# Optimization experiments

Measured on AMD Instinct MI355X. Metric: run time of the kernel, lower is better.

## Reference

```python
import jax, jax.numpy as jnp
import numpy as np

B, F, T, D, O = 8192, 512, 64, 6, 128
N_INTERNAL = 2 ** D - 1  # 63
N_LEAVES = 2 ** D        # 64


def smooth_step(t):
    tc = jnp.clip(t, -0.5, 0.5)
    return -2.0 * tc ** 3 + 1.5 * tc + 0.5


def setup_inputs() -> dict:
    key = jax.random.key(0)
    k1, k2, k3, k4 = jax.random.split(key, 4)
    x = jax.random.normal(k1, (B, F), dtype=jnp.float32)
    # Stacked per-node Linear weights in BFS (heap) order: node i -> row i.
    W_nodes = jax.random.normal(k2, (N_INTERNAL, F, T), dtype=jnp.float32) * (1.0 / np.sqrt(F))
    b_nodes = jax.random.normal(k3, (N_INTERNAL, T), dtype=jnp.float32) * 0.01
    # Per-leaf mixing weight [out_features, num_trees], leaves in BFS order.
    W_leaf = jax.random.normal(k4, (N_LEAVES, O, T), dtype=jnp.float32)
    return {"x": x, "W_nodes": W_nodes, "b_nodes": b_nodes, "W_leaf": W_leaf}


def reference(x, W_nodes, b_nodes, W_leaf):
    n_internal = W_nodes.shape[0]
    depth = int(np.log2(n_internal + 1))
    # All internal-node gates in one stacked GEMM: [B, n_internal, T]
    s = smooth_step(jnp.einsum('bf,nft->bnt', x, W_nodes) + b_nodes[None, :, :])
    b, _, t = s.shape
    prob = jnp.ones((b, 1, t), dtype=s.dtype)  # root prob
    start = 0
    for lvl in range(depth):
        width = 2 ** lvl
        s_l = s[:, start:start + width]  # [B, width, T], nodes at this level
        start += width
        # node local j -> children local 2j (left, prob*s) and 2j+1 (right, prob*(1-s))
        prob = jnp.stack([prob * s_l, prob * (1.0 - s_l)], axis=2).reshape(b, 2 * width, t)
    # prob: [B, n_leaves, T]; mix per-leaf, per-tree weights -> [B, O]
    out = jnp.einsum('blt,lot->bo', prob, W_leaf)
    return out
```

## Files before the change

kernel.cpp:

```cpp
#include <hip/hip_runtime.h>
#include <hip/hip_fp16.h>

#define BATCH 8192
#define FDIM  512
#define NTREE 64
#define NODES 63
#define ODIM  128
#define NJP   4096
#define K2    4096
#define TPG   8

typedef _Float16 f16;
typedef _Float16 f16x2 __attribute__((ext_vector_type(2)));
typedef _Float16 f16x8 __attribute__((ext_vector_type(8)));
typedef float    f32x4 __attribute__((ext_vector_type(4)));

#define XH_OFF   0
#define XH_SZ    ((size_t)BATCH*FDIM*2)
#define WNH_OFF  (XH_OFF + XH_SZ)
#define WNH_SZ   ((size_t)NJP*FDIM*2)
#define WLT_OFF  (WNH_OFF + WNH_SZ)
#define WLT_SZ   ((size_t)ODIM*K2*2)
#define PS_OFF   (WLT_OFF + WLT_SZ)
#define PS_SZ    ((size_t)TPG*BATCH*ODIM*4)
#define WS_NEEDED (PS_OFF + PS_SZ)

__device__ __forceinline__ float smooth_step_f(float t) {
    float tc = fminf(fmaxf(t, -0.5f), 0.5f);
    return fmaf(tc, fmaf(-2.0f * tc, tc, 1.5f), 0.5f);
}

__device__ __forceinline__ void async16(const void* g, void* l) {
    __builtin_amdgcn_global_load_lds((__attribute__((address_space(1))) void*)g,
                                     (__attribute__((address_space(3))) void*)l,
                                     16, 0, 0);
}

__device__ __forceinline__ int sw_off(int row, int g) {
    return ((row >> 3) * 512) + (((row & 7) * 8 + (g ^ (row & 7))) * 8);
}

__global__ void conv_x_kernel(const float* __restrict__ in, f16* __restrict__ out) {
    size_t i = ((size_t)blockIdx.x * blockDim.x + threadIdx.x) * 4;
    float4 v = *(const float4*)(in + i);
    f16* o = out + i;
    o[0] = (f16)v.x; o[1] = (f16)v.y; o[2] = (f16)v.z; o[3] = (f16)v.w;
}

__global__ void conv_wl_kernel(const float* __restrict__ in, f16* __restrict__ out) {
    __shared__ f16 tile[64][72];
    const int o    = blockIdx.x;
    const int lane = threadIdx.x & 63;
    const int w    = threadIdx.x >> 6;
    #pragma unroll
    for (int lc = 0; lc < 16; ++lc) {
        int l = w * 16 + lc;
        tile[lane][l] = (f16)in[(size_t)l * (ODIM * NTREE) + o * 64 + lane];
    }
    __syncthreads();
    f16* orow = out + (size_t)o * K2;
    #pragma unroll
    for (int c = 0; c < 2; ++c) {
        int idx = (threadIdx.x * 2 + c) * 8;
        int t = idx >> 6, l = idx & 63;
        f16x8 v;
        #pragma unroll
        for (int e = 0; e < 8; ++e) v[e] = tile[t][l + e];
        *(f16x8*)(orow + idx) = v;
    }
}

__global__ void conv_wn_kernel(const float* __restrict__ wn, f16* __restrict__ out) {
    const int n    = blockIdx.x;
    const int f0   = blockIdx.y * 64;
    const int lane = threadIdx.x & 63;
    const int w    = threadIdx.x >> 6;
    if (n == NODES) {
        #pragma unroll
        for (int tc = 0; tc < 16; ++tc) {
            int t = w * 16 + tc;
            out[(size_t)(t * 64 + NODES) * FDIM + f0 + lane] = (f16)0.0f;
        }
        return;
    }
    __shared__ float tile[64][65];
    const float* src = wn + (size_t)n * (FDIM * NTREE);
    #pragma unroll
    for (int i = 0; i < 16; ++i) {
        int fl = w * 16 + i;
        tile[fl][lane] = src[(size_t)(f0 + fl) * NTREE + lane];
    }
    __syncthreads();
    #pragma unroll
    for (int i = 0; i < 16; ++i) {
        int t = w * 16 + i;
        out[(size_t)(t * 64 + n) * FDIM + f0 + lane] = (f16)tile[lane][t];
    }
}

__global__ __launch_bounds__(256, 2)
void fused_tree(const f16* __restrict__ xh, const f16* __restrict__ wnh,
                const float* __restrict__ bn, const f16* __restrict__ wlt,
                float* __restrict__ partial)
{
    __shared__ f16 SH[33024];
    f16* CT = SH + 16384;
    const int tid  = threadIdx.x;
    const int lane = tid & 63;
    const int w    = tid >> 6;
    const int wm   = w & 1;
    const int wn   = w >> 1;
    const int row0 = blockIdx.x * 128;
    const int tpg  = blockIdx.y;

    const int lr = lane >> 3;
    const int lg = (lane & 7) ^ lr;
    const int frow = tid & 127;
    const int ftr  = tid >> 7;

    f32x4 lacc[4][4] = {};

    for (int tpi = 0; tpi < 4; ++tpi) {
        const int tp = tpg * 4 + tpi;
        const int j0 = tp * 128;

        f32x4 acc[4][4] = {};
        for (int k0 = 0; k0 < FDIM; k0 += 64) {
            #pragma unroll
            for (int q = 0; q < 8; ++q) {
                int id = w * 8 + q;
                if (id < 16) {
                    int r = id * 8 + lr;
                    async16(xh + (size_t)(row0 + r) * FDIM + k0 + lg * 8, &SH[id * 512 + lane * 8]);
                } else {
                    int c = id - 16;
                    int r = c * 8 + lr;
                    async16(wnh + (size_t)(j0 + r) * FDIM + k0 + lg * 8, &SH[8192 + c * 512 + lane * 8]);
                }
            }
            __syncthreads();
            #pragma unroll
            for (int ks = 0; ks < 2; ++ks) {
                int g = ks * 4 + (lane >> 4);
                f16x8 bfr[4];
                #pragma unroll
                for (int tn = 0; tn < 4; ++tn) {
                    int j = wn * 64 + tn * 16 + (lane & 15);
                    bfr[tn] = *(const f16x8*)&SH[8192 + sw_off(j, g)];
                }
                #pragma unroll
                for (int tm = 0; tm < 4; ++tm) {
                    int m = wm * 64 + tm * 16 + (lane & 15);
                    f16x8 afr = *(const f16x8*)&SH[sw_off(m, g)];
                    #pragma unroll
                    for (int tn = 0; tn < 4; ++tn)
                        acc[tm][tn] = __builtin_amdgcn_mfma_f32_16x16x32_f16(afr, bfr[tn], acc[tm][tn], 0, 0, 0);
                }
            }
            __syncthreads();
        }

        #pragma unroll
        for (int q = 0; q < 8; ++q) {
            int id = w * 8 + q;
            int h = id >> 4, c = id & 15;
            int o = c * 8 + lr;
            async16(wlt + (size_t)o * K2 + j0 + h * 64 + lg * 8,
                    &SH[h * 8192 + c * 512 + lane * 8]);
        }

        #pragma unroll
        for (int tn = 0; tn < 4; ++tn) {
            int col = wn * 64 + tn * 16 + (lane & 15);
            int nn  = col & 63;
            int tt  = (j0 + col) >> 6;
            float bias = (nn < NODES) ? bn[nn * NTREE + tt] : 0.0f;
            #pragma unroll
            for (int tm = 0; tm < 4; ++tm) {
                #pragma unroll
                for (int r = 0; r < 4; ++r) {
                    int row = wm * 64 + tm * 16 + (lane >> 4) * 4 + r;
                    CT[row * 130 + col] = (f16)smooth_step_f(acc[tm][tn][r] + bias);
                }
            }
        }
        __syncthreads();

        f16x8 ov[8];
        {
            const f16* gp = &CT[frow * 130 + ftr * 64];
            float g[64];
            #pragma unroll
            for (int c = 0; c < 32; ++c) {
                f16x2 v = *(const f16x2*)(gp + 2 * c);
                g[2 * c]     = (float)v[0];
                g[2 * c + 1] = (float)v[1];
            }
            float pr[32];
            pr[0] = 1.0f;
            int bse = 0;
            #pragma unroll
            for (int lvl = 0; lvl < 5; ++lvl) {
                const int width = 1 << lvl;
                #pragma unroll
                for (int i = width - 1; i >= 0; --i) {
                    float p = pr[i], s = g[bse + i];
                    pr[2 * i]     = p * s;
                    pr[2 * i + 1] = p * (1.0f - s);
                }
                bse += width;
            }
            #pragma unroll
            for (int i = 0; i < 32; ++i) {
                float s5 = g[31 + i];
                float p  = pr[i];
                ov[i >> 2][(i & 3) * 2]     = (f16)(p * s5);
                ov[i >> 2][(i & 3) * 2 + 1] = (f16)(p * (1.0f - s5));
            }
        }
        __syncthreads();

        #pragma unroll
        for (int g2 = 0; g2 < 8; ++g2)
            *(f16x8*)&SH[16384 + ftr * 8192 + sw_off(frow, g2)] = ov[g2];
        __syncthreads();

        #pragma unroll
        for (int ks2 = 0; ks2 < 4; ++ks2) {
            int h  = ks2 >> 1;
            int gg = (ks2 & 1) * 4 + (lane >> 4);
            f16x8 bfr[4];
            #pragma unroll
            for (int tn = 0; tn < 4; ++tn) {
                int o = wn * 64 + tn * 16 + (lane & 15);
                bfr[tn] = *(const f16x8*)&SH[h * 8192 + sw_off(o, gg)];
            }
            #pragma unroll
            for (int tm = 0; tm < 4; ++tm) {
                int m = wm * 64 + tm * 16 + (lane & 15);
                f16x8 afr = *(const f16x8*)&SH[16384 + h * 8192 + sw_off(m, gg)];
                #pragma unroll
                for (int tn = 0; tn < 4; ++tn)
                    lacc[tm][tn] = __builtin_amdgcn_mfma_f32_16x16x32_f16(afr, bfr[tn], lacc[tm][tn], 0, 0, 0);
            }
        }
        __syncthreads();
    }

    float* dst = partial + (size_t)tpg * BATCH * ODIM;
    #pragma unroll
    for (int tn = 0; tn < 4; ++tn) {
        int o = wn * 64 + tn * 16 + (lane & 15);
        #pragma unroll
        for (int tm = 0; tm < 4; ++tm) {
            #pragma unroll
            for (int r = 0; r < 4; ++r) {
                int row = row0 + wm * 64 + tm * 16 + (lane >> 4) * 4 + r;
                dst[(size_t)row * ODIM + o] = lacc[tm][tn][r];
            }
        }
    }
}

__global__ void reduce_kernel(const float* __restrict__ partial, float* __restrict__ out) {
    size_t i = ((size_t)blockIdx.x * blockDim.x + threadIdx.x) * 4;
    f32x4 a = *(const f32x4*)(partial + i);
    #pragma unroll
    for (int k = 1; k < TPG; ++k)
        a += *(const f32x4*)(partial + (size_t)k * BATCH * ODIM + i);
    *(f32x4*)(out + i) = a;
}

#define ROWS 8
__global__ __launch_bounds__(256, 2)
void soft_tree_fallback(const float* __restrict__ x, const float* __restrict__ Wn,
                        const float* __restrict__ bn, const float* __restrict__ Wl,
                        float* __restrict__ out)
{
    __shared__ __half s_lds[ROWS][NODES][NTREE];
    const int lane = threadIdx.x & 63;
    const int w    = threadIdx.x >> 6;
    const long row0 = (long)blockIdx.x * ROWS;
    for (int n = w; n < NODES; n += 4) {
        const float* wp = Wn + ((long)n * FDIM) * NTREE + lane;
        const float* xp = x + row0 * FDIM;
        float acc[ROWS];
        #pragma unroll
        for (int r = 0; r < ROWS; ++r) acc[r] = 0.0f;
        #pragma unroll 8
        for (int f = 0; f < FDIM; ++f) {
            float wv = wp[(long)f * NTREE];
            #pragma unroll
            for (int r = 0; r < ROWS; ++r)
                acc[r] = fmaf(xp[r * FDIM + f], wv, acc[r]);
        }
        float bias = bn[n * NTREE + lane];
        #pragma unroll
        for (int r = 0; r < ROWS; ++r)
            s_lds[r][n][lane] = __float2half(smooth_step_f(acc[r] + bias));
    }
    __syncthreads();
    const int r0 = w * 2, r1 = w * 2 + 1;
    float pr0[64], pr1[64];
    {
        pr0[0] = 1.0f; pr1[0] = 1.0f;
        int base = 0;
        #pragma unroll
        for (int lvl = 0; lvl < 6; ++lvl) {
            const int width = 1 << lvl;
            #pragma unroll
            for (int i = width - 1; i >= 0; --i) {
                float sa = __half2float(s_lds[r0][base + i][lane]);
                float sb = __half2float(s_lds[r1][base + i][lane]);
                float pa = pr0[i], pb = pr1[i];
                pr0[2 * i] = pa * sa; pr0[2 * i + 1] = pa * (1.0f - sa);
                pr1[2 * i] = pb * sb; pr1[2 * i + 1] = pb * (1.0f - sb);
            }
            base += width;
        }
    }
    for (int o = 0; o < ODIM; ++o) {
        const float* wlp = Wl + (long)o * NTREE + lane;
        float c0 = 0.0f, c1 = 0.0f;
        #pragma unroll
        for (int l = 0; l < 64; ++l) {
            float wv = wlp[(long)l * (ODIM * NTREE)];
            c0 = fmaf(pr0[l], wv, c0);
            c1 = fmaf(pr1[l], wv, c1);
        }
        #pragma unroll
        for (int off = 32; off > 0; off >>= 1) {
            c0 += __shfl_xor(c0, off, 64);
            c1 += __shfl_xor(c1, off, 64);
        }
        if (lane == 0) {
            out[(row0 + r0) * ODIM + o] = c0;
            out[(row0 + r1) * ODIM + o] = c1;
        }
    }
}

extern "C" void kernel_launch(void* const* d_in, const int* in_sizes, int n_in,
                              void* d_out, int out_size, void* d_ws, size_t ws_size,
                              hipStream_t stream) {
    const float* x  = (const float*)d_in[0];
    const float* Wn = (const float*)d_in[1];
    const float* bn = (const float*)d_in[2];
    const float* Wl = (const float*)d_in[3];
    float* out = (float*)d_out;

    if (ws_size < WS_NEEDED) {
        soft_tree_fallback<<<BATCH / ROWS, 256, 0, stream>>>(x, Wn, bn, Wl, out);
        return;
    }

    f16*   xh  = (f16*)((char*)d_ws + XH_OFF);
    f16*   wnh = (f16*)((char*)d_ws + WNH_OFF);
    f16*   wlt = (f16*)((char*)d_ws + WLT_OFF);
    float* ps  = (float*)((char*)d_ws + PS_OFF);

    conv_x_kernel <<<(BATCH * FDIM) / (256 * 4), 256, 0, stream>>>(x, xh);
    conv_wl_kernel<<<ODIM, 256, 0, stream>>>(Wl, wlt);
    conv_wn_kernel<<<dim3(64, FDIM / 64), 256, 0, stream>>>(Wn, wnh);

    fused_tree<<<dim3(BATCH / 128, TPG), 256, 0, stream>>>(xh, wnh, bn, wlt, ps);
    reduce_kernel<<<(BATCH * ODIM) / (256 * 4), 256, 0, stream>>>(ps, out);
}
```

Measured before the change: 160.1 us.

## Merge conversion kernels and replace partial-sum reduction with atomic accumulation

Folds the three fp16 conversion kernels into a single prep kernel that picks its role from the block index, cutting launch count. Drops the TPG partial-sum buffer and the separate reduce kernel: fused_tree now atomically adds its tile results into a zeroed output. This removes the 32 MB partial write and read-back plus one launch. In exchange it adds a memset and 8-way atomic contention per output element, and the summation order is no longer deterministic.

```diff
diff --git a/kernel.cpp b/kernel.cpp
--- a/kernel.cpp
+++ b/kernel.cpp
@@ -21,9 +21,7 @@
 #define WNH_SZ   ((size_t)NJP*FDIM*2)
 #define WLT_OFF  (WNH_OFF + WNH_SZ)
 #define WLT_SZ   ((size_t)ODIM*K2*2)
-#define PS_OFF   (WLT_OFF + WLT_SZ)
-#define PS_SZ    ((size_t)TPG*BATCH*ODIM*4)
-#define WS_NEEDED (PS_OFF + PS_SZ)
+#define WS_NEEDED (WLT_OFF + WLT_SZ)
 
 __device__ __forceinline__ float smooth_step_f(float t) {
     float tc = fminf(fmaxf(t, -0.5f), 0.5f);
@@ -40,68 +38,80 @@
     return ((row >> 3) * 512) + (((row & 7) * 8 + (g ^ (row & 7))) * 8);
 }
 
-__global__ void conv_x_kernel(const float* __restrict__ in, f16* __restrict__ out) {
-    size_t i = ((size_t)blockIdx.x * blockDim.x + threadIdx.x) * 4;
-    float4 v = *(const float4*)(in + i);
-    f16* o = out + i;
-    o[0] = (f16)v.x; o[1] = (f16)v.y; o[2] = (f16)v.z; o[3] = (f16)v.w;
-}
-
-__global__ void conv_wl_kernel(const float* __restrict__ in, f16* __restrict__ out) {
-    __shared__ f16 tile[64][72];
-    const int o    = blockIdx.x;
-    const int lane = threadIdx.x & 63;
-    const int w    = threadIdx.x >> 6;
-    #pragma unroll
-    for (int lc = 0; lc < 16; ++lc) {
-        int l = w * 16 + lc;
-        tile[lane][l] = (f16)in[(size_t)l * (ODIM * NTREE) + o * 64 + lane];
-    }
-    __syncthreads();
-    f16* orow = out + (size_t)o * K2;
-    #pragma unroll
-    for (int c = 0; c < 2; ++c) {
-        int idx = (threadIdx.x * 2 + c) * 8;
-        int t = idx >> 6, l = idx & 63;
-        f16x8 v;
-        #pragma unroll
-        for (int e = 0; e < 8; ++e) v[e] = tile[t][l + e];
-        *(f16x8*)(orow + idx) = v;
-    }
-}
-
-__global__ void conv_wn_kernel(const float* __restrict__ wn, f16* __restrict__ out) {
-    const int n    = blockIdx.x;
-    const int f0   = blockIdx.y * 64;
-    const int lane = threadIdx.x & 63;
-    const int w    = threadIdx.x >> 6;
-    if (n == NODES) {
-        #pragma unroll
-        for (int tc = 0; tc < 16; ++tc) {
-            int t = w * 16 + tc;
-            out[(size_t)(t * 64 + NODES) * FDIM + f0 + lane] = (f16)0.0f;
-        }
+#define XBLK 4096
+#define WLBLK 128
+__global__ __launch_bounds__(256)
+void prep_kernel(const float* __restrict__ x, const float* __restrict__ wn,
+                 const float* __restrict__ wl,
+                 f16* __restrict__ xh, f16* __restrict__ wnh, f16* __restrict__ wlt)
+{
+    __shared__ __align__(16) char smem[16640];
+    const int bid = blockIdx.x;
+
+    if (bid < XBLK) {
+        size_t i = ((size_t)bid * 256 + threadIdx.x) * 4;
+        float4 v = *(const float4*)(x + i);
+        f16* o = xh + i;
+        o[0] = (f16)v.x; o[1] = (f16)v.y; o[2] = (f16)v.z; o[3] = (f16)v.w;
         return;
     }
-    __shared__ float tile[64][65];
-    const float* src = wn + (size_t)n * (FDIM * NTREE);
-    #pragma unroll
-    for (int i = 0; i < 16; ++i) {
-        int fl = w * 16 + i;
-        tile[fl][lane] = src[(size_t)(f0 + fl) * NTREE + lane];
-    }
-    __syncthreads();
-    #pragma unroll
-    for (int i = 0; i < 16; ++i) {
-        int t = w * 16 + i;
-        out[(size_t)(t * 64 + n) * FDIM + f0 + lane] = (f16)tile[lane][t];
+    if (bid < XBLK + WLBLK) {
+        f16 (*tile)[72] = (f16(*)[72])smem;
+        const int o    = bid - XBLK;
+        const int lane = threadIdx.x & 63;
+        const int w    = threadIdx.x >> 6;
+        #pragma unroll
+        for (int lc = 0; lc < 16; ++lc) {
+            int l = w * 16 + lc;
+            tile[lane][l] = (f16)wl[(size_t)l * (ODIM * NTREE) + o * 64 + lane];
+        }
+        __syncthreads();
+        f16* orow = wlt + (size_t)o * K2;
+        #pragma unroll
+        for (int c = 0; c < 2; ++c) {
+            int idx = (threadIdx.x * 2 + c) * 8;
+            int t = idx >> 6, l = idx & 63;
+            f16x8 v;
+            #pragma unroll
+            for (int e = 0; e < 8; ++e) v[e] = tile[t][l + e];
+            *(f16x8*)(orow + idx) = v;
+        }
+        return;
+    }
+    {
+        const int id   = bid - (XBLK + WLBLK);
+        const int n    = id & 63;
+        const int f0   = (id >> 6) * 64;
+        const int lane = threadIdx.x & 63;
+        const int w    = threadIdx.x >> 6;
+        if (n == NODES) {
+            #pragma unroll
+            for (int tc = 0; tc < 16; ++tc) {
+                int t = w * 16 + tc;
+                wnh[(size_t)(t * 64 + NODES) * FDIM + f0 + lane] = (f16)0.0f;
+            }
+            return;
+        }
+        float (*tile)[65] = (float(*)[65])smem;
+        const float* src = wn + (size_t)n * (FDIM * NTREE);
+        #pragma unroll
+        for (int i = 0; i < 16; ++i) {
+            int fl = w * 16 + i;
+            tile[fl][lane] = src[(size_t)(f0 + fl) * NTREE + lane];
+        }
+        __syncthreads();
+        #pragma unroll
+        for (int i = 0; i < 16; ++i) {
+            int t = w * 16 + i;
+            wnh[(size_t)(t * 64 + n) * FDIM + f0 + lane] = (f16)tile[lane][t];
+        }
     }
 }
 
 __global__ __launch_bounds__(256, 2)
 void fused_tree(const f16* __restrict__ xh, const f16* __restrict__ wnh,
                 const float* __restrict__ bn, const f16* __restrict__ wlt,
-                float* __restrict__ partial)
+                float* __restrict__ out)
 {
     __shared__ f16 SH[33024];
     f16* CT = SH + 16384;
@@ -247,7 +257,6 @@
         __syncthreads();
     }
 
-    float* dst = partial + (size_t)tpg * BATCH * ODIM;
     #pragma unroll
     for (int tn = 0; tn < 4; ++tn) {
         int o = wn * 64 + tn * 16 + (lane & 15);
@@ -256,19 +265,10 @@
             #pragma unroll
             for (int r = 0; r < 4; ++r) {
                 int row = row0 + wm * 64 + tm * 16 + (lane >> 4) * 4 + r;
-                dst[(size_t)row * ODIM + o] = lacc[tm][tn][r];
-            }
-        }
-    }
-}
-
-__global__ void reduce_kernel(const float* __restrict__ partial, float* __restrict__ out) {
-    size_t i = ((size_t)blockIdx.x * blockDim.x + threadIdx.x) * 4;
-    f32x4 a = *(const f32x4*)(partial + i);
-    #pragma unroll
-    for (int k = 1; k < TPG; ++k)
-        a += *(const f32x4*)(partial + (size_t)k * BATCH * ODIM + i);
-    *(f32x4*)(out + i) = a;
+                atomicAdd(&out[(size_t)row * ODIM + o], lacc[tm][tn][r]);
+            }
+        }
+    }
 }
 
 #define ROWS 8
@@ -354,15 +354,11 @@
         return;
     }
 
-    f16*   xh  = (f16*)((char*)d_ws + XH_OFF);
-    f16*   wnh = (f16*)((char*)d_ws + WNH_OFF);
-    f16*   wlt = (f16*)((char*)d_ws + WLT_OFF);
-    float* ps  = (float*)((char*)d_ws + PS_OFF);
-
-    conv_x_kernel <<<(BATCH * FDIM) / (256 * 4), 256, 0, stream>>>(x, xh);
-    conv_wl_kernel<<<ODIM, 256, 0, stream>>>(Wl, wlt);
-    conv_wn_kernel<<<dim3(64, FDIM / 64), 256, 0, stream>>>(Wn, wnh);
-
-    fused_tree<<<dim3(BATCH / 128, TPG), 256, 0, stream>>>(xh, wnh, bn, wlt, ps);
-    reduce_kernel<<<(BATCH * ODIM) / (256 * 4), 256, 0, stream>>>(ps, out);
-}
+    f16* xh  = (f16*)((char*)d_ws + XH_OFF);
+    f16* wnh = (f16*)((char*)d_ws + WNH_OFF);
+    f16* wlt = (f16*)((char*)d_ws + WLT_OFF);
+
+    hipMemsetAsync(d_out, 0, (size_t)out_size * sizeof(float), stream);
+    prep_kernel<<<XBLK + WLBLK + 512, 256, 0, stream>>>(x, Wn, Wl, xh, wnh, wlt);
+    fused_tree<<<dim3(BATCH / 128, TPG), 256, 0, stream>>>(xh, wnh, bn, wlt, out);
+}
```

Result: slower. 166.9 us (+4.2%).
